# Performance work log

Measured on AMD Instinct MI355X. Metric: run time of the kernel, lower is better.

## Reference

```python
import jax, jax.numpy as jnp
import numpy as np


def _entmax15(x, axis=-1):
    # Faithful port of Entmax15Function (alpha=1.5 entmax, closed-form via sort).
    x = x - jnp.max(x, axis=axis, keepdims=True)  # numerical stability
    x = x / 2.0                                   # alpha=1.5 rescaling
    d = x.shape[axis]
    # sort descending along axis
    xsrt = -jnp.sort(-x, axis=axis)
    shape = [1] * x.ndim
    shape[axis] = d
    rho = jnp.arange(1, d + 1, dtype=x.dtype).reshape(shape)
    mean = jnp.cumsum(xsrt, axis=axis) / rho
    mean_sq = jnp.cumsum(xsrt * xsrt, axis=axis) / rho
    ss = rho * (mean_sq - mean * mean)
    delta = (1.0 - ss) / rho
    delta_nz = jnp.maximum(delta, 0.0)
    tau = mean - jnp.sqrt(delta_nz)
    # support size: number of sorted entries with tau <= xsrt
    support_size = jnp.sum((tau <= xsrt).astype(jnp.int32), axis=axis, keepdims=True)
    tau_star = jnp.take_along_axis(tau, support_size - 1, axis=axis)
    y = jnp.maximum(x - tau_star, 0.0)
    return y * y


def setup_inputs() -> dict:
    key = jax.random.key(0)
    x = jax.random.normal(key, (4096, 32000), dtype=jnp.float32)
    return {"x": x}


def reference(x) -> jnp.ndarray:
    return _entmax15(x, axis=-1)
```

## Files before the change

kernel.cpp:

```cpp
#include <hip/hip_runtime.h>
#include <math.h>


#define ROWLEN 32000
#define ROWV4  8000
#define BLOCK  256
#define NWAVE  4
#define NV     31
#define SEGCAP 768

typedef float f32x4 __attribute__((ext_vector_type(4)));

__global__ __launch_bounds__(BLOCK, 3)
void entmax15_kernel(const float* __restrict__ x, float* __restrict__ out,
                     int rows) {
  const int row = blockIdx.x;
  if (row >= rows) return;
  const int t    = threadIdx.x;
  const int lane = t & 63;
  const int wid  = t >> 6;

  __shared__ float s_wmax[NWAVE];
  __shared__ int   s_cnt[NWAVE];
  __shared__ float s_tau;
  __shared__ float s_seg[NWAVE][SEGCAP];

  const f32x4* __restrict__ xr = (const f32x4*)(x + (size_t)row * ROWLEN);

  f32x4 v[NV];
  f32x4 vtail;
#pragma unroll
  for (int i = 0; i < NV; ++i) v[i] = xr[i * BLOCK + t];
  vtail = xr[(t < 64) ? (NV * BLOCK + t) : t];

  float lmax = -1e30f;
#pragma unroll
  for (int i = 0; i < NV; ++i)
    lmax = fmaxf(lmax, fmaxf(fmaxf(v[i].x, v[i].y), fmaxf(v[i].z, v[i].w)));
  lmax = fmaxf(lmax, fmaxf(fmaxf(vtail.x, vtail.y), fmaxf(vtail.z, vtail.w)));
#pragma unroll
  for (int m = 32; m >= 1; m >>= 1) lmax = fmaxf(lmax, __shfl_xor(lmax, m));
  const float thr = lmax - 2.0f;

  int c = 0;
#pragma unroll
  for (int i = 0; i < NV; ++i)
    c += (v[i].x > thr) + (v[i].y > thr) + (v[i].z > thr) + (v[i].w > thr);
  if (t < 64)
    c += (vtail.x > thr) + (vtail.y > thr) + (vtail.z > thr) + (vtail.w > thr);

  int incl = c;
#pragma unroll
  for (int m = 1; m < 64; m <<= 1) {
    int nb = __shfl_up(incl, m);
    if (lane >= m) incl += nb;
  }

  {
    float* seg = &s_seg[wid][0];
    int off = incl - c;
    float a;
#pragma unroll
    for (int i = 0; i < NV; ++i) {
      a = v[i].x; if (a > thr) { if (off < SEGCAP) seg[off] = a; ++off; }
      a = v[i].y; if (a > thr) { if (off < SEGCAP) seg[off] = a; ++off; }
      a = v[i].z; if (a > thr) { if (off < SEGCAP) seg[off] = a; ++off; }
      a = v[i].w; if (a > thr) { if (off < SEGCAP) seg[off] = a; ++off; }
    }
    if (t < 64) {
      a = vtail.x; if (a > thr) { if (off < SEGCAP) seg[off] = a; ++off; }
      a = vtail.y; if (a > thr) { if (off < SEGCAP) seg[off] = a; ++off; }
      a = vtail.z; if (a > thr) { if (off < SEGCAP) seg[off] = a; ++off; }
      a = vtail.w; if (a > thr) { if (off < SEGCAP) seg[off] = a; ++off; }
    }
  }
  if (lane == 63) {
    s_cnt[wid]  = min(incl, SEGCAP);
    s_wmax[wid] = lmax;
  }
  __syncthreads();

  if (wid == 0) {
    float xmax = fmaxf(fmaxf(s_wmax[0], s_wmax[1]),
                       fmaxf(s_wmax[2], s_wmax[3]));
    float tau = -1.0f;
    for (int it = 0; it < 6; ++it) {
      float s = 0.f, q = 0.f;
#pragma unroll 1
      for (int w2 = 0; w2 < NWAVE; ++w2) {
        const int cnt = s_cnt[w2];
        const float* sg = &s_seg[w2][0];
        for (int j = lane; j < cnt; j += 64) {
          float d = fmaf(sg[j] - xmax, 0.5f, -tau);
          if (d > 0.f) { s += d; q += d * d; }
        }
      }
#pragma unroll
      for (int m = 32; m >= 1; m >>= 1) {
        s += __shfl_xor(s, m);
        q += __shfl_xor(q, m);
      }
      if (s > 0.f) tau += (q - 1.0f) / (2.0f * s);
    }
    for (int it = 0; it < 2; ++it) {
      float kk = 0.f, s1 = 0.f, s2 = 0.f;
#pragma unroll 1
      for (int w2 = 0; w2 < NWAVE; ++w2) {
        const int cnt = s_cnt[w2];
        const float* sg = &s_seg[w2][0];
        for (int j = lane; j < cnt; j += 64) {
          float z = (sg[j] - xmax) * 0.5f;
          if (z > tau) { kk += 1.f; s1 += z; s2 += z * z; }
        }
      }
#pragma unroll
      for (int m = 32; m >= 1; m >>= 1) {
        kk += __shfl_xor(kk, m);
        s1 += __shfl_xor(s1, m);
        s2 += __shfl_xor(s2, m);
      }
      float disc = s1 * s1 - kk * (s2 - 1.0f);
      tau = (s1 - sqrtf(fmaxf(disc, 0.f))) / kk;
    }
    if (lane == 0) s_tau = fmaf(xmax, 0.5f, tau);
  }
  __syncthreads();
  const float cc = s_tau;

  f32x4* __restrict__ outr = (f32x4*)(out + (size_t)row * ROWLEN);
  float d;
#pragma unroll
  for (int i = 0; i < NV; ++i) {
    f32x4 o;
    d = fmaf(v[i].x, 0.5f, -cc); o.x = d > 0.f ? d * d : 0.f;
    d = fmaf(v[i].y, 0.5f, -cc); o.y = d > 0.f ? d * d : 0.f;
    d = fmaf(v[i].z, 0.5f, -cc); o.z = d > 0.f ? d * d : 0.f;
    d = fmaf(v[i].w, 0.5f, -cc); o.w = d > 0.f ? d * d : 0.f;
    outr[i * BLOCK + t] = o;
  }
  if (t < 64) {
    f32x4 o;
    d = fmaf(vtail.x, 0.5f, -cc); o.x = d > 0.f ? d * d : 0.f;
    d = fmaf(vtail.y, 0.5f, -cc); o.y = d > 0.f ? d * d : 0.f;
    d = fmaf(vtail.z, 0.5f, -cc); o.z = d > 0.f ? d * d : 0.f;
    d = fmaf(vtail.w, 0.5f, -cc); o.w = d > 0.f ? d * d : 0.f;
    outr[NV * BLOCK + t] = o;
  }
}

extern "C" void kernel_launch(void* const* d_in, const int* in_sizes, int n_in,
                              void* d_out, int out_size, void* d_ws, size_t ws_size,
                              hipStream_t stream) {
  const float* x = (const float*)d_in[0];
  float* out = (float*)d_out;
  int rows = in_sizes[0] / ROWLEN;
  hipLaunchKernelGGL(entmax15_kernel, dim3(rows), dim3(BLOCK), 0, stream,
                     x, out, rows);
}
```

Measured before the change: 234.3 us.

## Keep only part of each row in registers and re-read the rest for higher occupancy

Only 20 of the 31 vector groups stay in registers. The other 11 are re-loaded from global memory twice: once for candidate compaction, which now uses wave ballots, and once when writing the output. The launch bound rises from 3 to 4 blocks per CU to raise occupancy and hide memory latency, at the cost of extra global reads, which should mostly hit cache. The threshold solver also gains one more iteration in each loop and does its final quadratic step in double precision, which adds a little serial work.

```diff
diff --git a/kernel.cpp b/kernel.cpp
--- a/kernel.cpp
+++ b/kernel.cpp
@@ -6,12 +6,13 @@
 #define ROWV4  8000
 #define BLOCK  256
 #define NWAVE  4
-#define NV     31
+#define NREG   20
+#define NGRP   31
 #define SEGCAP 768
 
 typedef float f32x4 __attribute__((ext_vector_type(4)));
 
-__global__ __launch_bounds__(BLOCK, 3)
+__global__ __launch_bounds__(BLOCK, 4)
 void entmax15_kernel(const float* __restrict__ x, float* __restrict__ out,
                      int rows) {
   const int row = blockIdx.x;
@@ -27,55 +28,82 @@
 
   const f32x4* __restrict__ xr = (const f32x4*)(x + (size_t)row * ROWLEN);
 
-  f32x4 v[NV];
-  f32x4 vtail;
-#pragma unroll
-  for (int i = 0; i < NV; ++i) v[i] = xr[i * BLOCK + t];
-  vtail = xr[(t < 64) ? (NV * BLOCK + t) : t];
-
+  f32x4 v[NREG];
+  f32x4 vt = {-1e30f, -1e30f, -1e30f, -1e30f};
   float lmax = -1e30f;
 #pragma unroll
-  for (int i = 0; i < NV; ++i)
+  for (int i = 0; i < NREG; ++i) {
+    v[i] = xr[i * BLOCK + t];
     lmax = fmaxf(lmax, fmaxf(fmaxf(v[i].x, v[i].y), fmaxf(v[i].z, v[i].w)));
-  lmax = fmaxf(lmax, fmaxf(fmaxf(vtail.x, vtail.y), fmaxf(vtail.z, vtail.w)));
+  }
+#pragma unroll
+  for (int i = NREG; i < NGRP; ++i) {
+    f32x4 u = xr[i * BLOCK + t];
+    lmax = fmaxf(lmax, fmaxf(fmaxf(u.x, u.y), fmaxf(u.z, u.w)));
+  }
+  if (t < 64) {
+    vt = xr[NGRP * BLOCK + t];
+    lmax = fmaxf(lmax, fmaxf(fmaxf(vt.x, vt.y), fmaxf(vt.z, vt.w)));
+  }
 #pragma unroll
   for (int m = 32; m >= 1; m >>= 1) lmax = fmaxf(lmax, __shfl_xor(lmax, m));
   const float thr = lmax - 2.0f;
 
   int c = 0;
 #pragma unroll
-  for (int i = 0; i < NV; ++i)
+  for (int i = 0; i < NREG; ++i)
     c += (v[i].x > thr) + (v[i].y > thr) + (v[i].z > thr) + (v[i].w > thr);
-  if (t < 64)
-    c += (vtail.x > thr) + (vtail.y > thr) + (vtail.z > thr) + (vtail.w > thr);
-
+  c += (vt.x > thr) + (vt.y > thr) + (vt.z > thr) + (vt.w > thr);
   int incl = c;
 #pragma unroll
   for (int m = 1; m < 64; m <<= 1) {
     int nb = __shfl_up(incl, m);
     if (lane >= m) incl += nb;
   }
-
+  float* seg = &s_seg[wid][0];
   {
-    float* seg = &s_seg[wid][0];
     int off = incl - c;
     float a;
 #pragma unroll
-    for (int i = 0; i < NV; ++i) {
+    for (int i = 0; i < NREG; ++i) {
       a = v[i].x; if (a > thr) { if (off < SEGCAP) seg[off] = a; ++off; }
       a = v[i].y; if (a > thr) { if (off < SEGCAP) seg[off] = a; ++off; }
       a = v[i].z; if (a > thr) { if (off < SEGCAP) seg[off] = a; ++off; }
       a = v[i].w; if (a > thr) { if (off < SEGCAP) seg[off] = a; ++off; }
     }
-    if (t < 64) {
-      a = vtail.x; if (a > thr) { if (off < SEGCAP) seg[off] = a; ++off; }
-      a = vtail.y; if (a > thr) { if (off < SEGCAP) seg[off] = a; ++off; }
-      a = vtail.z; if (a > thr) { if (off < SEGCAP) seg[off] = a; ++off; }
-      a = vtail.w; if (a > thr) { if (off < SEGCAP) seg[off] = a; ++off; }
+    a = vt.x; if (a > thr) { if (off < SEGCAP) seg[off] = a; ++off; }
+    a = vt.y; if (a > thr) { if (off < SEGCAP) seg[off] = a; ++off; }
+    a = vt.z; if (a > thr) { if (off < SEGCAP) seg[off] = a; ++off; }
+    a = vt.w; if (a > thr) { if (off < SEGCAP) seg[off] = a; ++off; }
+  }
+  int base = __shfl(incl, 63);
+  const unsigned long long lmask = (1ull << lane) - 1ull;
+#pragma unroll
+  for (int i = NREG; i < NGRP; ++i) {
+    f32x4 u = xr[i * BLOCK + t];
+    {
+      bool p = u.x > thr; unsigned long long m = __ballot(p);
+      if (p) { int ix = base + (int)__popcll(m & lmask); if (ix < SEGCAP) seg[ix] = u.x; }
+      base += (int)__popcll(m);
+    }
+    {
+      bool p = u.y > thr; unsigned long long m = __ballot(p);
+      if (p) { int ix = base + (int)__popcll(m & lmask); if (ix < SEGCAP) seg[ix] = u.y; }
+      base += (int)__popcll(m);
+    }
+    {
+      bool p = u.z > thr; unsigned long long m = __ballot(p);
+      if (p) { int ix = base + (int)__popcll(m & lmask); if (ix < SEGCAP) seg[ix] = u.z; }
+      base += (int)__popcll(m);
+    }
+    {
+      bool p = u.w > thr; unsigned long long m = __ballot(p);
+      if (p) { int ix = base + (int)__popcll(m & lmask); if (ix < SEGCAP) seg[ix] = u.w; }
+      base += (int)__popcll(m);
     }
   }
-  if (lane == 63) {
-    s_cnt[wid]  = min(incl, SEGCAP);
+  if (lane == 0) {
+    s_cnt[wid]  = min(base, SEGCAP);
     s_wmax[wid] = lmax;
   }
   __syncthreads();
@@ -84,15 +112,15 @@
     float xmax = fmaxf(fmaxf(s_wmax[0], s_wmax[1]),
                        fmaxf(s_wmax[2], s_wmax[3]));
     float tau = -1.0f;
-    for (int it = 0; it < 6; ++it) {
+    for (int it = 0; it < 7; ++it) {
       float s = 0.f, q = 0.f;
 #pragma unroll 1
       for (int w2 = 0; w2 < NWAVE; ++w2) {
         const int cnt = s_cnt[w2];
         const float* sg = &s_seg[w2][0];
         for (int j = lane; j < cnt; j += 64) {
-          float d = fmaf(sg[j] - xmax, 0.5f, -tau);
-          if (d > 0.f) { s += d; q += d * d; }
+          float dd = fmaf(sg[j] - xmax, 0.5f, -tau);
+          if (dd > 0.f) { s += dd; q += dd * dd; }
         }
       }
 #pragma unroll
@@ -102,7 +130,7 @@
       }
       if (s > 0.f) tau += (q - 1.0f) / (2.0f * s);
     }
-    for (int it = 0; it < 2; ++it) {
+    for (int it = 0; it < 3; ++it) {
       float kk = 0.f, s1 = 0.f, s2 = 0.f;
 #pragma unroll 1
       for (int w2 = 0; w2 < NWAVE; ++w2) {
@@ -119,8 +147,10 @@
         s1 += __shfl_xor(s1, m);
         s2 += __shfl_xor(s2, m);
       }
-      float disc = s1 * s1 - kk * (s2 - 1.0f);
-      tau = (s1 - sqrtf(fmaxf(disc, 0.f))) / kk;
+      double dk = (double)kk, d1 = (double)s1, d2 = (double)s2;
+      double disc = d1 * d1 - dk * (d2 - 1.0);
+      disc = disc > 0.0 ? disc : 0.0;
+      tau = (float)((d1 - sqrt(disc)) / dk);
     }
     if (lane == 0) s_tau = fmaf(xmax, 0.5f, tau);
   }
@@ -130,7 +160,7 @@
   f32x4* __restrict__ outr = (f32x4*)(out + (size_t)row * ROWLEN);
   float d;
 #pragma unroll
-  for (int i = 0; i < NV; ++i) {
+  for (int i = 0; i < NREG; ++i) {
     f32x4 o;
     d = fmaf(v[i].x, 0.5f, -cc); o.x = d > 0.f ? d * d : 0.f;
     d = fmaf(v[i].y, 0.5f, -cc); o.y = d > 0.f ? d * d : 0.f;
@@ -138,13 +168,23 @@
     d = fmaf(v[i].w, 0.5f, -cc); o.w = d > 0.f ? d * d : 0.f;
     outr[i * BLOCK + t] = o;
   }
+#pragma unroll
+  for (int i = NREG; i < NGRP; ++i) {
+    f32x4 u = xr[i * BLOCK + t];
+    f32x4 o;
+    d = fmaf(u.x, 0.5f, -cc); o.x = d > 0.f ? d * d : 0.f;
+    d = fmaf(u.y, 0.5f, -cc); o.y = d > 0.f ? d * d : 0.f;
+    d = fmaf(u.z, 0.5f, -cc); o.z = d > 0.f ? d * d : 0.f;
+    d = fmaf(u.w, 0.5f, -cc); o.w = d > 0.f ? d * d : 0.f;
+    outr[i * BLOCK + t] = o;
+  }
   if (t < 64) {
     f32x4 o;
-    d = fmaf(vtail.x, 0.5f, -cc); o.x = d > 0.f ? d * d : 0.f;
-    d = fmaf(vtail.y, 0.5f, -cc); o.y = d > 0.f ? d * d : 0.f;
-    d = fmaf(vtail.z, 0.5f, -cc); o.z = d > 0.f ? d * d : 0.f;
-    d = fmaf(vtail.w, 0.5f, -cc); o.w = d > 0.f ? d * d : 0.f;
-    outr[NV * BLOCK + t] = o;
+    d = fmaf(vt.x, 0.5f, -cc); o.x = d > 0.f ? d * d : 0.f;
+    d = fmaf(vt.y, 0.5f, -cc); o.y = d > 0.f ? d * d : 0.f;
+    d = fmaf(vt.z, 0.5f, -cc); o.z = d > 0.f ? d * d : 0.f;
+    d = fmaf(vt.w, 0.5f, -cc); o.w = d > 0.f ? d * d : 0.f;
+    outr[NGRP * BLOCK + t] = o;
   }
 }
 
```

After: 294.0 us. 25.5% more time.
